# Optimization experiments

Measured on AMD Instinct MI355X. Metric: run time of the kernel, lower is better.

Reference implementation:

```python
import jax, jax.numpy as jnp
import numpy as np

B, LQ, LK, D = 8, 2048, 2048, 128

def setup_inputs() -> dict:
    key = jax.random.key(0)
    k1, k2, k3, k4 = jax.random.split(key, 4)
    return {
        "query": jax.random.normal(k1, (B, LQ, D), dtype=jnp.float32),
        "key": jax.random.normal(k2, (B, LK, D), dtype=jnp.float32),
        "value": jax.random.normal(k3, (B, LK, D), dtype=jnp.float32),
        "scale_factor": jax.random.normal(k4, (B, LQ, LK), dtype=jnp.float32),
    }

def reference(query, key, value, scale_factor):
    # qk: [B, LQ, LK]
    qk = jnp.einsum("bqd,bkd->bqk", query, key)
    probs = jax.nn.softmax(qk * scale_factor, axis=-1)
    # dropout_p = 0.0 -> identity
    return jnp.einsum("bqk,bkd->bqd", probs, value)
```

## Files before the change

### kernel.cpp

```cpp
#include <hip/hip_runtime.h>
#include <hip/hip_bf16.h>


typedef float          f32x4 __attribute__((ext_vector_type(4)));
typedef short          s16x8 __attribute__((ext_vector_type(8)));
typedef unsigned int   u32x4 __attribute__((ext_vector_type(4)));
typedef unsigned short u16x4 __attribute__((ext_vector_type(4)));

#define LOG2E 1.4426950408889634f

__device__ __forceinline__ float fast_exp2(float x) {
#if __has_builtin(__builtin_amdgcn_exp2f)
    return __builtin_amdgcn_exp2f(x);
#else
    return exp2f(x);
#endif
}

__device__ __forceinline__ unsigned short f2bf(float x) {
    return __builtin_bit_cast(unsigned short, __float2bfloat16(x));
}
__device__ __forceinline__ float bf2f(unsigned short u) {
    return __bfloat162float(__builtin_bit_cast(__hip_bfloat16, u));
}

__global__ void conv_split(const float* __restrict__ src,
                           unsigned short* __restrict__ hi,
                           unsigned short* __restrict__ lo, int n4) {
    int i = blockIdx.x * blockDim.x + threadIdx.x;
    if (i >= n4) return;
    const float4 v = ((const float4*)src)[i];
    float f[4] = {v.x, v.y, v.z, v.w};
    u16x4 h, l;
#pragma unroll
    for (int j = 0; j < 4; ++j) {
        unsigned short hb = f2bf(f[j]);
        h[j] = hb;
        l[j] = f2bf(f[j] - bf2f(hb));
    }
    ((u16x4*)hi)[i] = h;
    ((u16x4*)lo)[i] = l;
}

__global__ void transpose_v(const float* __restrict__ v,
                            unsigned short* __restrict__ vt) {
    __shared__ unsigned short tile[64 * 132];
    const int b   = blockIdx.x & 7;
    const int k0  = (blockIdx.x >> 3) * 64;
    const int tid = threadIdx.x;
#pragma unroll
    for (int p = 0; p < 8; ++p) {
        int idx  = p * 256 + tid;
        int k    = idx >> 5;
        int dblk = idx & 31;
        float4 val = ((const float4*)v)[((b * 2048 + k0 + k) * 128 + dblk * 4) >> 2];
        u16x4 t4;
        t4[0] = f2bf(val.x); t4[1] = f2bf(val.y);
        t4[2] = f2bf(val.z); t4[3] = f2bf(val.w);
        *(u16x4*)&tile[k * 132 + dblk * 4] = t4;
    }
    __syncthreads();
#pragma unroll
    for (int p = 0; p < 4; ++p) {
        int idx = p * 256 + tid;
        int d   = idx >> 3;
        int k8  = idx & 7;
        u16x4 a, c;
#pragma unroll
        for (int j = 0; j < 4; ++j) a[j] = tile[(k8 * 8 + j) * 132 + d];
#pragma unroll
        for (int j = 0; j < 4; ++j) c[j] = tile[(k8 * 8 + 4 + j) * 132 + d];
        unsigned short* outp = vt + (b * 128 + d) * 2048 + k0 + k8 * 8;
        *(u16x4*)outp       = a;
        *(u16x4*)(outp + 4) = c;
    }
}

#define KHS 136
#define VTS 72
#define PS  72

__global__ __launch_bounds__(256, 2)
void flash_fwd(const unsigned short* __restrict__ qh_g,
               const unsigned short* __restrict__ ql_g,
               const unsigned short* __restrict__ kh_g,
               const unsigned short* __restrict__ kl_g,
               const unsigned short* __restrict__ vt_g,
               const float* __restrict__ scale_g,
               float* __restrict__ opart,
               float* __restrict__ mpart,
               float* __restrict__ lpart) {
    __shared__ unsigned short lds_kh[64 * KHS];
    __shared__ unsigned short lds_kl[64 * KHS];
    __shared__ unsigned short lds_vt[128 * VTS];
    __shared__ unsigned short lds_p[4][16 * PS];

    const int tid  = threadIdx.x;
    const int wave = tid >> 6;
    const int lane = tid & 63;
    const int c    = lane & 15;
    const int g    = lane >> 4;

    const int bid   = blockIdx.x;
    const int b     = bid & 7;
    const int qt    = (bid >> 3) & 31;
    const int ks    = bid >> 8;
    const int q0    = qt * 64;
    const int kbase = ks * 1024;

    const int srow = tid >> 4, sc8 = tid & 15;
    const int sdv  = tid >> 3, sk8 = tid & 7;

    s16x8 qh[4], ql[4];
    {
        const int qrow = b * 2048 + q0 + wave * 16 + c;
#pragma unroll
        for (int kstep = 0; kstep < 4; ++kstep) {
            int idx = qrow * 16 + kstep * 4 + g;
            qh[kstep] = __builtin_bit_cast(s16x8, ((const u32x4*)qh_g)[idx]);
            ql[kstep] = __builtin_bit_cast(s16x8, ((const u32x4*)ql_g)[idx]);
        }
    }

    f32x4 oacc[8];
#pragma unroll
    for (int t = 0; t < 8; ++t) oacc[t] = (f32x4){0.f, 0.f, 0.f, 0.f};
    float m2[4], ln[4];
#pragma unroll
    for (int r = 0; r < 4; ++r) { m2[r] = -INFINITY; ln[r] = 0.f; }

    u32x4 pk[4], pl[4], pv[4];
    float scn[4][4];
    const int scb = (b * 2048 + q0 + wave * 16 + g * 4) * 2048 + c;

    {
        const int k0 = kbase;
#pragma unroll
        for (int p = 0; p < 4; ++p) {
            int gidx = (b * 2048 + k0 + p * 16 + srow) * 16 + sc8;
            pk[p] = ((const u32x4*)kh_g)[gidx];
            pl[p] = ((const u32x4*)kl_g)[gidx];
            int vidx = (b * 128 + p * 32 + sdv) * 256 + (k0 >> 3) + sk8;
            pv[p] = ((const u32x4*)vt_g)[vidx];
        }
#pragma unroll
        for (int t = 0; t < 4; ++t)
#pragma unroll
            for (int r = 0; r < 4; ++r)
                scn[t][r] = scale_g[scb + r * 2048 + k0 + t * 16];
    }

    for (int kc = 0; kc < 16; ++kc) {
        const int k0 = kbase + kc * 64;

        __syncthreads();
#pragma unroll
        for (int p = 0; p < 4; ++p) {
            *(u32x4*)&lds_kh[(p * 16 + srow) * KHS + sc8 * 8] = pk[p];
            *(u32x4*)&lds_kl[(p * 16 + srow) * KHS + sc8 * 8] = pl[p];
            *(u32x4*)&lds_vt[(p * 32 + sdv) * VTS + sk8 * 8]  = pv[p];
        }
        __syncthreads();

        float sc[4][4];
#pragma unroll
        for (int t = 0; t < 4; ++t)
#pragma unroll
            for (int r = 0; r < 4; ++r)
                sc[t][r] = scn[t][r] * LOG2E;

        if (kc < 15) {
            const int kn = k0 + 64;
#pragma unroll
            for (int p = 0; p < 4; ++p) {
                int gidx = (b * 2048 + kn + p * 16 + srow) * 16 + sc8;
                pk[p] = ((const u32x4*)kh_g)[gidx];
                pl[p] = ((const u32x4*)kl_g)[gidx];
                int vidx = (b * 128 + p * 32 + sdv) * 256 + (kn >> 3) + sk8;
                pv[p] = ((const u32x4*)vt_g)[vidx];
            }
#pragma unroll
            for (int t = 0; t < 4; ++t)
#pragma unroll
                for (int r = 0; r < 4; ++r)
                    scn[t][r] = scale_g[scb + r * 2048 + kn + t * 16];
        }

        f32x4 s[4];
#pragma unroll
        for (int t = 0; t < 4; ++t) s[t] = (f32x4){0.f, 0.f, 0.f, 0.f};
#pragma unroll
        for (int kstep = 0; kstep < 4; ++kstep) {
#pragma unroll
            for (int t = 0; t < 4; ++t) {
                int off = (t * 16 + c) * KHS + kstep * 32 + g * 8;
                s16x8 bh = *(const s16x8*)&lds_kh[off];
                s16x8 bl = *(const s16x8*)&lds_kl[off];
                s[t] = __builtin_amdgcn_mfma_f32_16x16x32_bf16(qh[kstep], bh, s[t], 0, 0, 0);
                s[t] = __builtin_amdgcn_mfma_f32_16x16x32_bf16(ql[kstep], bh, s[t], 0, 0, 0);
                s[t] = __builtin_amdgcn_mfma_f32_16x16x32_bf16(qh[kstep], bl, s[t], 0, 0, 0);
            }
        }

        float lt[4][4], mx[4];
#pragma unroll
        for (int r = 0; r < 4; ++r) {
            lt[0][r] = s[0][r] * sc[0][r];
            lt[1][r] = s[1][r] * sc[1][r];
            lt[2][r] = s[2][r] * sc[2][r];
            lt[3][r] = s[3][r] * sc[3][r];
            mx[r] = fmaxf(fmaxf(lt[0][r], lt[1][r]), fmaxf(lt[2][r], lt[3][r]));
        }
#pragma unroll
        for (int mask = 1; mask < 16; mask <<= 1)
#pragma unroll
            for (int r = 0; r < 4; ++r)
                mx[r] = fmaxf(mx[r], __shfl_xor(mx[r], mask));
        float al[4], rs[4];
#pragma unroll
        for (int r = 0; r < 4; ++r) {
            float mn = fmaxf(m2[r], mx[r]);
            al[r] = fast_exp2(m2[r] - mn);
            m2[r] = mn;
            rs[r] = 0.f;
        }
#pragma unroll
        for (int t = 0; t < 4; ++t)
#pragma unroll
            for (int r = 0; r < 4; ++r) {
                float p = fast_exp2(lt[t][r] - m2[r]);
                rs[r] += p;
                lds_p[wave][(g * 4 + r) * PS + t * 16 + c] = f2bf(p);
            }
#pragma unroll
        for (int mask = 1; mask < 16; mask <<= 1)
#pragma unroll
            for (int r = 0; r < 4; ++r)
                rs[r] += __shfl_xor(rs[r], mask);
#pragma unroll
        for (int r = 0; r < 4; ++r) ln[r] = ln[r] * al[r] + rs[r];
#pragma unroll
        for (int t = 0; t < 8; ++t)
#pragma unroll
            for (int r = 0; r < 4; ++r) oacc[t][r] *= al[r];

#pragma unroll
        for (int k2 = 0; k2 < 2; ++k2) {
            s16x8 af = *(const s16x8*)&lds_p[wave][c * PS + k2 * 32 + g * 8];
#pragma unroll
            for (int t2 = 0; t2 < 8; ++t2) {
                s16x8 bv = *(const s16x8*)&lds_vt[(t2 * 16 + c) * VTS + k2 * 32 + g * 8];
                oacc[t2] = __builtin_amdgcn_mfma_f32_16x16x32_bf16(af, bv, oacc[t2], 0, 0, 0);
            }
        }
    }

    {
        const int rowb = (ks * 8 + b) * 2048 + q0 + wave * 16;
#pragma unroll
        for (int t2 = 0; t2 < 8; ++t2)
#pragma unroll
            for (int r = 0; r < 4; ++r)
                opart[(rowb + g * 4 + r) * 128 + t2 * 16 + c] = oacc[t2][r];
        if (c == 0) {
#pragma unroll
            for (int r = 0; r < 4; ++r) {
                mpart[rowb + g * 4 + r] = m2[r];
                lpart[rowb + g * 4 + r] = ln[r];
            }
        }
    }
}

__global__ void merge_halves(const float* __restrict__ opart,
                             const float* __restrict__ mpart,
                             const float* __restrict__ lpart,
                             float* __restrict__ out) {
    const int row = blockIdx.x;
    const int d   = threadIdx.x;
    const float m0 = mpart[row],  m1 = mpart[16384 + row];
    const float l0 = lpart[row],  l1 = lpart[16384 + row];
    const float M  = fmaxf(m0, m1);
    const float a0 = fast_exp2(m0 - M);
    const float a1 = fast_exp2(m1 - M);
    const float inv = 1.f / (a0 * l0 + a1 * l1);
    const int i = row * 128 + d;
    out[i] = (a0 * opart[i] + a1 * opart[16384 * 128 + i]) * inv;
}

extern "C" void kernel_launch(void* const* d_in, const int* in_sizes, int n_in,
                              void* d_out, int out_size, void* d_ws, size_t ws_size,
                              hipStream_t stream) {
    const float* q  = (const float*)d_in[0];
    const float* k  = (const float*)d_in[1];
    const float* v  = (const float*)d_in[2];
    const float* sc = (const float*)d_in[3];
    float* out = (float*)d_out;

    char* ws = (char*)d_ws;
    const size_t MB = 1024 * 1024;
    unsigned short* qh = (unsigned short*)(ws);
    unsigned short* ql = (unsigned short*)(ws + 4 * MB);
    unsigned short* kh = (unsigned short*)(ws + 8 * MB);
    unsigned short* kl = (unsigned short*)(ws + 12 * MB);
    unsigned short* vt = (unsigned short*)(ws + 16 * MB);
    float* opart = (float*)(ws + 20 * MB);
    float* mpart = (float*)(ws + 36 * MB);
    float* lpart = (float*)(ws + 36 * MB + 128 * 1024);

    conv_split<<<2048, 256, 0, stream>>>(q, qh, ql, 524288);
    conv_split<<<2048, 256, 0, stream>>>(k, kh, kl, 524288);
    transpose_v<<<256, 256, 0, stream>>>(v, vt);
    flash_fwd<<<512, 256, 0, stream>>>(qh, ql, kh, kl, vt, sc, opart, mpart, lpart);
    merge_halves<<<16384, 128, 0, stream>>>(opart, mpart, lpart, out);
}
```

Baseline: 253.6 us.

## Merge prep kernels and read V fragments directly from global in flash kernel

The three preprocessing launches (Q split, K split, V transpose) become one kernel with block-range dispatch, saving launch overhead. In the attention kernel, the LDS staging buffer for transposed V is removed and each wave loads its V MFMA operands straight from global memory just before the PV MFMAs. Launch bounds rise to 3 blocks per CU to use the freed LDS and raise occupancy. The trade-off is that V loads are no longer prefetched or shared across waves, so global load latency sits right before the MFMAs and each wave re-reads V redundantly through cache.

```diff
diff --git a/kernel.cpp b/kernel.cpp
--- a/kernel.cpp
+++ b/kernel.cpp
@@ -24,40 +24,51 @@
     return __bfloat162float(__builtin_bit_cast(__hip_bfloat16, u));
 }
 
-__global__ void conv_split(const float* __restrict__ src,
-                           unsigned short* __restrict__ hi,
-                           unsigned short* __restrict__ lo, int n4) {
-    int i = blockIdx.x * blockDim.x + threadIdx.x;
-    if (i >= n4) return;
-    const float4 v = ((const float4*)src)[i];
-    float f[4] = {v.x, v.y, v.z, v.w};
-    u16x4 h, l;
-#pragma unroll
-    for (int j = 0; j < 4; ++j) {
-        unsigned short hb = f2bf(f[j]);
-        h[j] = hb;
-        l[j] = f2bf(f[j] - bf2f(hb));
-    }
-    ((u16x4*)hi)[i] = h;
-    ((u16x4*)lo)[i] = l;
-}
-
-__global__ void transpose_v(const float* __restrict__ v,
-                            unsigned short* __restrict__ vt) {
+__global__ void prep(const float* __restrict__ q,
+                     const float* __restrict__ k,
+                     const float* __restrict__ v,
+                     unsigned short* __restrict__ qh,
+                     unsigned short* __restrict__ ql,
+                     unsigned short* __restrict__ kh,
+                     unsigned short* __restrict__ kl,
+                     unsigned short* __restrict__ vt) {
     __shared__ unsigned short tile[64 * 132];
-    const int b   = blockIdx.x & 7;
-    const int k0  = (blockIdx.x >> 3) * 64;
+    const int bb  = blockIdx.x;
     const int tid = threadIdx.x;
+
+    if (bb < 4096) {
+        const bool isq = bb < 2048;
+        const float* src = isq ? q : k;
+        unsigned short* hi = isq ? qh : kh;
+        unsigned short* lo = isq ? ql : kl;
+        const int i = (isq ? bb : bb - 2048) * 256 + tid;
+        const float4 val = ((const float4*)src)[i];
+        float f[4] = {val.x, val.y, val.z, val.w};
+        u16x4 h, l;
+#pragma unroll
+        for (int j = 0; j < 4; ++j) {
+            unsigned short hb = f2bf(f[j]);
+            h[j] = hb;
+            l[j] = f2bf(f[j] - bf2f(hb));
+        }
+        ((u16x4*)hi)[i] = h;
+        ((u16x4*)lo)[i] = l;
+        return;
+    }
+
+    const int tb = bb - 4096;
+    const int b  = tb & 7;
+    const int k0 = (tb >> 3) * 64;
 #pragma unroll
     for (int p = 0; p < 8; ++p) {
         int idx  = p * 256 + tid;
-        int k    = idx >> 5;
+        int kk   = idx >> 5;
         int dblk = idx & 31;
-        float4 val = ((const float4*)v)[((b * 2048 + k0 + k) * 128 + dblk * 4) >> 2];
+        float4 val = ((const float4*)v)[((b * 2048 + k0 + kk) * 128 + dblk * 4) >> 2];
         u16x4 t4;
         t4[0] = f2bf(val.x); t4[1] = f2bf(val.y);
         t4[2] = f2bf(val.z); t4[3] = f2bf(val.w);
-        *(u16x4*)&tile[k * 132 + dblk * 4] = t4;
+        *(u16x4*)&tile[kk * 132 + dblk * 4] = t4;
     }
     __syncthreads();
 #pragma unroll
@@ -77,10 +88,9 @@
 }
 
 #define KHS 136
-#define VTS 72
 #define PS  72
 
-__global__ __launch_bounds__(256, 2)
+__global__ __launch_bounds__(256, 3)
 void flash_fwd(const unsigned short* __restrict__ qh_g,
                const unsigned short* __restrict__ ql_g,
                const unsigned short* __restrict__ kh_g,
@@ -92,7 +102,6 @@
                float* __restrict__ lpart) {
     __shared__ unsigned short lds_kh[64 * KHS];
     __shared__ unsigned short lds_kl[64 * KHS];
-    __shared__ unsigned short lds_vt[128 * VTS];
     __shared__ unsigned short lds_p[4][16 * PS];
 
     const int tid  = threadIdx.x;
@@ -109,7 +118,6 @@
     const int kbase = ks * 1024;
 
     const int srow = tid >> 4, sc8 = tid & 15;
-    const int sdv  = tid >> 3, sk8 = tid & 7;
 
     s16x8 qh[4], ql[4];
     {
@@ -129,7 +137,7 @@
 #pragma unroll
     for (int r = 0; r < 4; ++r) { m2[r] = -INFINITY; ln[r] = 0.f; }
 
-    u32x4 pk[4], pl[4], pv[4];
+    u32x4 pk[4], pl[4];
     float scn[4][4];
     const int scb = (b * 2048 + q0 + wave * 16 + g * 4) * 2048 + c;
 
@@ -140,8 +148,6 @@
             int gidx = (b * 2048 + k0 + p * 16 + srow) * 16 + sc8;
             pk[p] = ((const u32x4*)kh_g)[gidx];
             pl[p] = ((const u32x4*)kl_g)[gidx];
-            int vidx = (b * 128 + p * 32 + sdv) * 256 + (k0 >> 3) + sk8;
-            pv[p] = ((const u32x4*)vt_g)[vidx];
         }
 #pragma unroll
         for (int t = 0; t < 4; ++t)
@@ -158,7 +164,6 @@
         for (int p = 0; p < 4; ++p) {
             *(u32x4*)&lds_kh[(p * 16 + srow) * KHS + sc8 * 8] = pk[p];
             *(u32x4*)&lds_kl[(p * 16 + srow) * KHS + sc8 * 8] = pl[p];
-            *(u32x4*)&lds_vt[(p * 32 + sdv) * VTS + sk8 * 8]  = pv[p];
         }
         __syncthreads();
 
@@ -176,8 +181,6 @@
                 int gidx = (b * 2048 + kn + p * 16 + srow) * 16 + sc8;
                 pk[p] = ((const u32x4*)kh_g)[gidx];
                 pl[p] = ((const u32x4*)kl_g)[gidx];
-                int vidx = (b * 128 + p * 32 + sdv) * 256 + (kn >> 3) + sk8;
-                pv[p] = ((const u32x4*)vt_g)[vidx];
             }
 #pragma unroll
             for (int t = 0; t < 4; ++t)
@@ -247,11 +250,14 @@
 #pragma unroll
         for (int k2 = 0; k2 < 2; ++k2) {
             s16x8 af = *(const s16x8*)&lds_p[wave][c * PS + k2 * 32 + g * 8];
-#pragma unroll
-            for (int t2 = 0; t2 < 8; ++t2) {
-                s16x8 bv = *(const s16x8*)&lds_vt[(t2 * 16 + c) * VTS + k2 * 32 + g * 8];
-                oacc[t2] = __builtin_amdgcn_mfma_f32_16x16x32_bf16(af, bv, oacc[t2], 0, 0, 0);
-            }
+            const int vb = (b * 128 + c) * 256 + (k0 >> 3) + k2 * 4 + g;
+            s16x8 bv[8];
+#pragma unroll
+            for (int t2 = 0; t2 < 8; ++t2)
+                bv[t2] = __builtin_bit_cast(s16x8, ((const u32x4*)vt_g)[vb + t2 * 4096]);
+#pragma unroll
+            for (int t2 = 0; t2 < 8; ++t2)
+                oacc[t2] = __builtin_amdgcn_mfma_f32_16x16x32_bf16(af, bv[t2], oacc[t2], 0, 0, 0);
         }
     }
 
@@ -308,9 +314,7 @@
     float* mpart = (float*)(ws + 36 * MB);
     float* lpart = (float*)(ws + 36 * MB + 128 * 1024);
 
-    conv_split<<<2048, 256, 0, stream>>>(q, qh, ql, 524288);
-    conv_split<<<2048, 256, 0, stream>>>(k, kh, kl, 524288);
-    transpose_v<<<256, 256, 0, stream>>>(v, vt);
+    prep<<<4352, 256, 0, stream>>>(q, k, v, qh, ql, kh, kl, vt);
     flash_fwd<<<512, 256, 0, stream>>>(qh, ql, kh, kl, vt, sc, opart, mpart, lpart);
     merge_halves<<<16384, 128, 0, stream>>>(opart, mpart, lpart, out);
 }
```

Result: slower. 298.9 us (+17.9%).
